# Kernel tuning notes

Measured on AMD Instinct MI355X. Metric: run time of the kernel, lower is better.

## Reference

```python
import jax, jax.numpy as jnp
import numpy as np
from jax.scipy.special import logsumexp

H = 128          # num_hidden_feature
L = 3            # num_layers (E3II/EGCL stack)
FL, FP = 16, 27  # ligand / pocket atom feature dims
NL, NP = 20000, 30000
EL, EP = 160000, 240000
B = 8            # graphs in the batch


def setup_inputs() -> dict:
    key = jax.random.key(0)
    ks = list(jax.random.split(key, 32))
    it = iter(ks)
    def rn(shape, s=0.05):
        return jax.random.normal(next(it), shape, jnp.float32) * s
    inp = {
        'ligand_x': jax.random.normal(next(it), (NL, FL), jnp.float32),
        'pocket_x': jax.random.normal(next(it), (NP, FP), jnp.float32),
        'ligand_pos': jax.random.normal(next(it), (NL, 3), jnp.float32),
        'pocket_pos': jax.random.normal(next(it), (NP, 3), jnp.float32),
        'Wl_emb': rn((FL, H)), 'bl_emb': rn((H,)),
        'Wp_emb': rn((FP, H)), 'bp_emb': rn((H,)),
        # per-layer EGCL params, stacked: axis0 = {0: ligand(l2l), 1: pocket(p2p)}, axis1 = layer
        'We1': rn((2, L, 2 * H + 1, H)), 'be1': rn((2, L, H)),
        'We2': rn((2, L, H, H)), 'be2': rn((2, L, H)),
        'Wx': rn((2, L, H, 1)), 'bx': rn((2, L, 1)),
        'Wh1': rn((2, L, 2 * H, H)), 'bh1': rn((2, L, H)),
        'Wh2': rn((2, L, H, H)), 'bh2': rn((2, L, H)),
        # NextType dense head: linspace(128,1,4) -> [128,85,43,1]
        'Wd1': rn((H, 85)), 'bd1': rn((85,)),
        'Wd2': rn((85, 43)), 'bd2': rn((43,)),
        'Wd3': rn((43, 1)), 'bd3': rn((1,)),
        'l2l_edge_index': jax.random.randint(next(it), (2, EL), 0, NL).astype(jnp.int32),
        'p2p_edge_index': jax.random.randint(next(it), (2, EP), 0, NP).astype(jnp.int32),
        'ligand_batch': jnp.sort(jax.random.randint(next(it), (NL,), 0, B)).astype(jnp.int32),
    }
    return inp


def _egcl(h, x, src, dst, We1, be1, We2, be2, Wx, bx, Wh1, bh1, Wh2, bh2):
    """One equivariant graph conv layer (gather -> edge MLP -> scatter)."""
    n = h.shape[0]
    rel = x[dst] - x[src]                                 # [E,3]
    d2 = jnp.sum(rel * rel, axis=-1, keepdims=True)        # [E,1]
    e_in = jnp.concatenate([h[dst], h[src], d2], axis=-1)  # [E,2H+1]
    m = jax.nn.silu(e_in @ We1 + be1)
    m = jax.nn.silu(m @ We2 + be2)                        # [E,H]
    coef = m @ Wx + bx                                     # [E,1]
    agg_x = jax.ops.segment_sum(rel * coef, dst, num_segments=n)
    deg = jax.ops.segment_sum(jnp.ones((dst.shape[0], 1), h.dtype), dst, num_segments=n)
    x = x + agg_x / jnp.maximum(deg, 1.0)                  # mean-normalized coord update
    agg_m = jax.ops.segment_sum(m, dst, num_segments=n)    # [N,H]
    upd = jax.nn.silu(jnp.concatenate([h, agg_m], axis=-1) @ Wh1 + bh1) @ Wh2 + bh2
    return h + upd, x


def reference(ligand_x, pocket_x, ligand_pos, pocket_pos,
              Wl_emb, bl_emb, Wp_emb, bp_emb,
              We1, be1, We2, be2, Wx, bx, Wh1, bh1, Wh2, bh2,
              Wd1, bd1, Wd2, bd2, Wd3, bd3,
              l2l_edge_index, p2p_edge_index, ligand_batch):
    # node embeddings (Embedding.l_node_emb / p_node_emb)
    hl = ligand_x @ Wl_emb + bl_emb
    hp = pocket_x @ Wp_emb + bp_emb
    xl, xp = ligand_pos, pocket_pos
    ls, ld = l2l_edge_index[0], l2l_edge_index[1]
    ps, pd = p2p_edge_index[0], p2p_edge_index[1]
    for l in range(L):
        hl, xl = _egcl(hl, xl, ls, ld, We1[0, l], be1[0, l], We2[0, l], be2[0, l],
                       Wx[0, l], bx[0, l], Wh1[0, l], bh1[0, l], Wh2[0, l], bh2[0, l])
        hp, xp = _egcl(hp, xp, ps, pd, We1[1, l], be1[1, l], We2[1, l], be2[1, l],
                       Wx[1, l], bx[1, l], Wh1[1, l], bh1[1, l], Wh2[1, l], bh2[1, l])
    # NextType head on ligand nodes: embedding(eye(FL)) == Wl_emb (+ bias)
    embed_type = Wl_emb + bl_emb                          # [FL,H]
    mul = embed_type[None, :, :] * hl[:, None, :]          # [NL,FL,H]
    t = jax.nn.silu(mul @ Wd1 + bd1)
    t = jax.nn.silu(t @ Wd2 + bd2)
    t = (t @ Wd3 + bd3)[..., 0]                            # [NL,FL]
    lg = jax.nn.log_softmax(t, axis=-1)
    agg = jax.ops.segment_sum(lg, ligand_batch, num_segments=B)  # [B,FL]
    return agg - logsumexp(agg, axis=-1, keepdims=True)
```

## Files before the change

kernel.cpp:

```cpp
#include <hip/hip_runtime.h>
#include <hip/hip_bf16.h>
#include <math.h>

typedef __attribute__((ext_vector_type(4))) float f4;
typedef __attribute__((ext_vector_type(4))) float f32x4;
typedef __attribute__((ext_vector_type(8))) short s8;
typedef __attribute__((ext_vector_type(4))) short s4;

#define H 128
#define NLAYERS 3
#define FLIG 16
#define FPOC 27
#define NLIG 20000
#define NPOC 30000
#define ELIG 160000
#define EPOC 240000
#define NB 8

#define EPB 128
#define NBLK_EL (ELIG/EPB)
#define NBLK_EP (EPOC/EPB)
#define NBLK_NL ((NLIG+31)/32)
#define NBLK_NP ((NPOC+31)/32)

#define G1S (8*8*64*8)
#define G2S (4*8*64*8)
#define W1FS (4*6*64*8)
#define WD2S (3*3*64*8)

__device__ __forceinline__ float silu_f(float v){
  return v * __builtin_amdgcn_rcpf(1.0f + __expf(-v));
}
__device__ __forceinline__ unsigned short f2bf(float v){
  __hip_bfloat16 b = __float2bfloat16(v);
  return *reinterpret_cast<unsigned short*>(&b);
}
__device__ __forceinline__ float bf2f(unsigned short u){
  unsigned int x = ((unsigned int)u) << 16;
  return __uint_as_float(x);
}
__device__ __forceinline__ int xcd_swz(int bid, int nwg){
  int q = nwg >> 3, r = nwg & 7;
  int x = bid & 7, w = bid >> 3;
  return (x < r) ? (x*(q+1) + w) : (r*(q+1) + (x-r)*q + w);
}

__global__ void k_embed2(const float* __restrict__ lx, const float* __restrict__ px,
                         const float* __restrict__ lpos, const float* __restrict__ ppos,
                         const float* __restrict__ Wl, const float* __restrict__ bl,
                         const float* __restrict__ Wp, const float* __restrict__ bp,
                         float* __restrict__ hl, unsigned short* __restrict__ hbl,
                         float* __restrict__ hp, unsigned short* __restrict__ hbp,
                         float* __restrict__ xl, float* __restrict__ xp){
  int bid = blockIdx.x;
  int g = (bid < NLIG/2) ? 0 : 1;
  int nb = (g ? bid - NLIG/2 : bid) * 2;
  const float* x  = g ? px : lx;
  const float* W  = g ? Wp : Wl;
  const float* b  = g ? bp : bl;
  float* h = g ? hp : hl;
  unsigned short* hb = g ? hbp : hbl;
  int F = g ? FPOC : FLIG;
  int tid = threadIdx.x;
  int n = nb + (tid >> 7);
  int j = tid & 127;
  float acc = b[j];
  for (int k = 0; k < F; k++) acc += x[n*F + k] * W[k*H + j];
  h[(size_t)n*H + j] = acc;
  hb[(size_t)n*H + j] = f2bf(acc);
  if (tid < 6){
    const float* pos = g ? ppos : lpos;
    float* xd = g ? xp : xl;
    xd[(size_t)nb*3 + tid] = pos[(size_t)nb*3 + tid];
  }
}

__global__ void k_hist2(const int* __restrict__ ldst, const int* __restrict__ pdst,
                        int* __restrict__ deg_l, int* __restrict__ deg_p){
  int e = blockIdx.x*256 + threadIdx.x;
  if (e < ELIG) atomicAdd(&deg_l[ldst[e]], 1);
  else if (e < ELIG+EPOC) atomicAdd(&deg_p[pdst[e-ELIG]], 1);
}

__global__ void k_scan2(const int* __restrict__ deg_l, int* __restrict__ offs_l,
                        const int* __restrict__ deg_p, int* __restrict__ offs_p){
  __shared__ int part[1024];
  const int* deg = blockIdx.x ? deg_p : deg_l;
  int* offs = blockIdx.x ? offs_p : offs_l;
  int N = blockIdx.x ? NPOC : NLIG;
  int E = blockIdx.x ? EPOC : ELIG;
  int t = threadIdx.x;
  int chunk = (N + 1023) >> 10;
  int b0 = t*chunk;
  int b1 = b0 + chunk; if (b1 > N) b1 = N;
  int s = 0;
  for (int i = b0; i < b1; i++) s += deg[i];
  part[t] = s;
  __syncthreads();
  for (int off = 1; off < 1024; off <<= 1){
    int v = (t >= off) ? part[t-off] : 0;
    __syncthreads();
    part[t] += v;
    __syncthreads();
  }
  int run = part[t] - s;
  for (int i = b0; i < b1; i++){ offs[i] = run; run += deg[i]; }
  if (t == 1023) offs[N] = E;
}

__global__ void k_sort2(const int* __restrict__ lsrc, const int* __restrict__ ldst,
                        const int* __restrict__ psrc, const int* __restrict__ pdst,
                        const int* __restrict__ offs_l, const int* __restrict__ offs_p,
                        int* __restrict__ cur_l, int* __restrict__ cur_p,
                        int* __restrict__ ssrc_l, int* __restrict__ sdst_l,
                        int* __restrict__ ssrc_p, int* __restrict__ sdst_p){
  int e = blockIdx.x*256 + threadIdx.x;
  if (e < ELIG){
    int d = ldst[e];
    int p = offs_l[d] + atomicAdd(&cur_l[d], 1);
    ssrc_l[p] = lsrc[e]; sdst_l[p] = d;
  } else if (e < ELIG+EPOC){
    int ee = e - ELIG;
    int d = pdst[ee];
    int p = offs_p[d] + atomicAdd(&cur_p[d], 1);
    ssrc_p[p] = psrc[ee]; sdst_p[p] = d;
  }
}

__global__ void k_pack(const float* __restrict__ We1, const float* __restrict__ We2,
                       const float* __restrict__ Wh1, const float* __restrict__ Wh2,
                       const float* __restrict__ Wl, const float* __restrict__ bl,
                       const float* __restrict__ Wd1, const float* __restrict__ Wd2,
                       unsigned short* __restrict__ We1p, unsigned short* __restrict__ We2p,
                       unsigned short* __restrict__ Wh1p, unsigned short* __restrict__ Wh2p,
                       unsigned short* __restrict__ W1p, unsigned short* __restrict__ Wd2p)
{
  int idx = blockIdx.x*256 + threadIdx.x;
  const int nWe1 = 6*G1S, nWe2 = 6*G2S, nWh1 = 6*G1S, nWh2 = 6*G2S, nW1 = 16*W1FS, nWd2 = WD2S;
  int i = idx;
  if (i < nWe1){
    int j = i&7, l = (i>>3)&63, t = (i>>9)&7, ks = (i>>12)&7, g = i>>15;
    int k = 32*ks + 8*(l>>4) + j, col = 16*t + (l&15);
    We1p[i] = f2bf(We1[((size_t)g*257 + k)*H + col]);
    return;
  }
  i -= nWe1;
  if (i < nWe2){
    int j = i&7, l = (i>>3)&63, t = (i>>9)&7, ks = (i>>12)&3, g = i>>14;
    int k = 32*ks + 8*(l>>4) + j, col = 16*t + (l&15);
    We2p[i] = f2bf(We2[((size_t)g*H + k)*H + col]);
    return;
  }
  i -= nWe2;
  if (i < nWh1){
    int j = i&7, l = (i>>3)&63, t = (i>>9)&7, ks = (i>>12)&7, g = i>>15;
    int k = 32*ks + 8*(l>>4) + j, col = 16*t + (l&15);
    Wh1p[i] = f2bf(Wh1[((size_t)g*256 + k)*H + col]);
    return;
  }
  i -= nWh1;
  if (i < nWh2){
    int j = i&7, l = (i>>3)&63, t = (i>>9)&7, ks = (i>>12)&3, g = i>>14;
    int k = 32*ks + 8*(l>>4) + j, col = 16*t + (l&15);
    Wh2p[i] = f2bf(Wh2[((size_t)g*H + k)*H + col]);
    return;
  }
  i -= nWh2;
  if (i < nW1){
    int f = i / W1FS, r = i % W1FS;
    int ks = r / (6*512), r2 = r % (6*512);
    int t = r2 / 512, l = (r2 % 512) >> 3, j = r2 & 7;
    int k = 32*ks + 8*(l>>4) + j, col = 16*t + (l&15);
    float v = 0.f;
    if (col < 85) v = (Wl[f*H + k] + bl[k]) * Wd1[k*85 + col];
    W1p[i] = f2bf(v);
    return;
  }
  i -= nW1;
  if (i < nWd2){
    int ks = i / (3*512), r2 = i % (3*512);
    int t = r2 / 512, l = (r2 % 512) >> 3, j = r2 & 7;
    int k = 32*ks + 8*(l>>4) + j, col = 16*t + (l&15);
    float v = 0.f;
    if (k < 85 && col < 43) v = Wd2[k*43 + col];
    Wd2p[i] = f2bf(v);
  }
}

__global__ __launch_bounds__(256, 3) void k_edge_f(
    const unsigned short* __restrict__ hb_l, const unsigned short* __restrict__ hb_p,
    const float* __restrict__ x_l, const float* __restrict__ x_p,
    const int* __restrict__ ssrc_l, const int* __restrict__ sdst_l,
    const int* __restrict__ ssrc_p, const int* __restrict__ sdst_p,
    const unsigned short* __restrict__ We1pb, const float* __restrict__ We1b,
    const float* __restrict__ be1b,
    const unsigned short* __restrict__ We2pb, const float* __restrict__ be2b,
    const float* __restrict__ Wxb, const float* __restrict__ bxb,
    unsigned short* __restrict__ m2e_l, float* __restrict__ relcf_l,
    unsigned short* __restrict__ m2e_p, float* __restrict__ relcf_p,
    int layer)
{
  __shared__ __align__(16) unsigned short m_lds[128*136];
  __shared__ float relS[128][3];
  __shared__ float d2S[128];
  __shared__ int sI[128], dI[128];
  unsigned short* m2t = m_lds;

  int tid = threadIdx.x;
  int bid = xcd_swz(blockIdx.x, NBLK_EL + NBLK_EP);
  int g = (bid < NBLK_EL) ? 0 : 1;
  int e0 = (g ? bid - NBLK_EL : bid) * EPB;
  const unsigned short* hb = g ? hb_p : hb_l;
  const float* x = g ? x_p : x_l;
  const int* ssrc = g ? ssrc_p : ssrc_l;
  const int* sdst = g ? sdst_p : sdst_l;
  unsigned short* m2e = g ? m2e_p : m2e_l;
  float* relcf = g ? relcf_p : relcf_l;
  int gl = g*NLAYERS + layer;
  const unsigned short* We1p = We1pb + (size_t)gl*G1S;
  const unsigned short* We2p = We2pb + (size_t)gl*G2S;
  const float* We1r256 = We1b + ((size_t)gl*257 + 256)*H;
  const float* be1 = be1b + (size_t)gl*H;
  const float* be2 = be2b + (size_t)gl*H;
  const float* Wx = Wxb + (size_t)gl*H;

  int lane = tid & 63, wave = tid >> 6;
  int c = lane & 15, q = lane >> 4;

  if (lane < 32){
    int e = wave*32 + lane;
    int s = ssrc[e0+e], d = sdst[e0+e];
    sI[e] = s; dI[e] = d;
    float rx = x[d*3+0]-x[s*3+0];
    float ry = x[d*3+1]-x[s*3+1];
    float rz = x[d*3+2]-x[s*3+2];
    relS[e][0]=rx; relS[e][1]=ry; relS[e][2]=rz;
    d2S[e] = rx*rx+ry*ry+rz*rz;
  }

  int eA = wave*32 + c;
  int eB = eA + 16;
  const unsigned short* pD0 = hb + (size_t)dI[eA]*H + q*8;
  const unsigned short* pS0 = hb + (size_t)sI[eA]*H + q*8;
  const unsigned short* pD1 = hb + (size_t)dI[eB]*H + q*8;
  const unsigned short* pS1 = hb + (size_t)sI[eB]*H + q*8;

  s8 af0[8], af1[8];
  #pragma unroll
  for (int ks=0; ks<4; ks++){
    af0[ks]   = *(const s8*)(pD0 + ks*32);
    af0[4+ks] = *(const s8*)(pS0 + ks*32);
    af1[ks]   = *(const s8*)(pD1 + ks*32);
    af1[4+ks] = *(const s8*)(pS1 + ks*32);
  }

  f32x4 acc0[8], acc1[8];
  #pragma unroll
  for (int t=0;t<8;t++){ acc0[t] = (f32x4){0.f,0.f,0.f,0.f}; acc1[t] = (f32x4){0.f,0.f,0.f,0.f}; }
  const s8* B1 = (const s8*)We1p;
  #pragma unroll
  for (int ks=0; ks<8; ks++){
    const s8* bp = B1 + (ks*8)*64 + lane;
    #pragma unroll
    for (int t=0;t<8;t++){
      s8 B = bp[t*64];
      acc0[t] = __builtin_amdgcn_mfma_f32_16x16x32_bf16(af0[ks], B, acc0[t], 0,0,0);
      acc1[t] = __builtin_amdgcn_mfma_f32_16x16x32_bf16(af1[ks], B, acc1[t], 0,0,0);
    }
  }

  int er0 = wave*32 + 4*q;
  int er1 = er0 + 16;
  float d20[4], d21[4];
  #pragma unroll
  for (int i=0;i<4;i++){ d20[i] = d2S[er0+i]; d21[i] = d2S[er1+i]; }
  #pragma unroll
  for (int t=0;t<8;t++){
    int j2 = 16*t + c;
    float w256 = We1r256[j2], bias = be1[j2];
    s4 mv0, mv1;
    #pragma unroll
    for (int i=0;i<4;i++){
      mv0[i] = (short)f2bf(silu_f(acc0[t][i] + d20[i]*w256 + bias));
      mv1[i] = (short)f2bf(silu_f(acc1[t][i] + d21[i]*w256 + bias));
    }
    *(s4*)&m_lds[136*j2 + er0] = mv0;
    *(s4*)&m_lds[136*j2 + er1] = mv1;
  }

  #pragma unroll
  for (int t=0;t<8;t++){ acc0[t] = (f32x4){0.f,0.f,0.f,0.f}; acc1[t] = (f32x4){0.f,0.f,0.f,0.f}; }
  const s8* B2 = (const s8*)We2p;
  #pragma unroll
  for (int ks=0; ks<4; ks++){
    s8 a20, a21;
    int base = 136*(32*ks + 8*q) + wave*32 + c;
    #pragma unroll
    for (int j=0;j<8;j++){
      a20[j] = (short)m_lds[base + 136*j];
      a21[j] = (short)m_lds[base + 16 + 136*j];
    }
    const s8* bp = B2 + (ks*8)*64 + lane;
    #pragma unroll
    for (int t=0;t<8;t++){
      s8 B = bp[t*64];
      acc0[t] = __builtin_amdgcn_mfma_f32_16x16x32_bf16(a20, B, acc0[t], 0,0,0);
      acc1[t] = __builtin_amdgcn_mfma_f32_16x16x32_bf16(a21, B, acc1[t], 0,0,0);
    }
  }
  __syncthreads();

  float pp0[4] = {0.f,0.f,0.f,0.f};
  float pp1[4] = {0.f,0.f,0.f,0.f};
  #pragma unroll
  for (int t=0;t<8;t++){
    int j2 = 16*t + c;
    float b2v = be2[j2], wxv = Wx[j2];
    #pragma unroll
    for (int i=0;i<4;i++){
      float v0 = silu_f(acc0[t][i] + b2v);
      float v1 = silu_f(acc1[t][i] + b2v);
      pp0[i] += v0*wxv;
      pp1[i] += v1*wxv;
      m2t[(er0+i)*136 + j2] = f2bf(v0);
      m2t[(er1+i)*136 + j2] = f2bf(v1);
    }
  }
  #pragma unroll
  for (int off=1; off<16; off<<=1){
    #pragma unroll
    for (int i=0;i<4;i++){
      pp0[i] += __shfl_xor(pp0[i], off, 64);
      pp1[i] += __shfl_xor(pp1[i], off, 64);
    }
  }
  if (c == 0){
    float bxv = bxb[gl];
    #pragma unroll
    for (int i=0;i<4;i++){
      int e = er0 + i;
      float cf = pp0[i] + bxv;
      float* rp = relcf + (size_t)(e0+e)*3;
      rp[0] = relS[e][0]*cf; rp[1] = relS[e][1]*cf; rp[2] = relS[e][2]*cf;
      e = er1 + i;
      cf = pp1[i] + bxv;
      rp = relcf + (size_t)(e0+e)*3;
      rp[0] = relS[e][0]*cf; rp[1] = relS[e][1]*cf; rp[2] = relS[e][2]*cf;
    }
  }

  {
    int e = wave*32 + (lane >> 1), cb = (lane & 1) * 64;
    const s8* sp = (const s8*)&m2t[e*136 + cb];
    s8* dp = (s8*)(m2e + (size_t)(e0+e)*H + cb);
    #pragma unroll
    for (int s2=0; s2<8; s2++) dp[s2] = sp[s2];
  }
}

__global__ __launch_bounds__(128, 4) void k_node_f(
    float* __restrict__ h_l, unsigned short* __restrict__ hb_l, float* __restrict__ x_l,
    float* __restrict__ h_p, unsigned short* __restrict__ hb_p, float* __restrict__ x_p,
    const unsigned short* __restrict__ m2e_l, const float* __restrict__ relcf_l,
    const unsigned short* __restrict__ m2e_p, const float* __restrict__ relcf_p,
    const int* __restrict__ offs_l, const int* __restrict__ offs_p,
    const unsigned short* __restrict__ Wh1pb, const float* __restrict__ bh1b,
    const unsigned short* __restrict__ Wh2pb, const float* __restrict__ bh2b,
    int layer)
{
  __shared__ __align__(16) unsigned short aggS[32*136];
  __shared__ __align__(16) unsigned short u_lds[128*36];
  __shared__ float rcS[32][3];
  __shared__ int degS[32];

  int tid = threadIdx.x;
  int bid = xcd_swz(blockIdx.x, NBLK_NL + NBLK_NP);
  int g = (bid < NBLK_NL) ? 0 : 1;
  int nb0 = (g ? bid - NBLK_NL : bid) * 32;
  int N = g ? NPOC : NLIG;
  float* h = g ? h_p : h_l;
  unsigned short* hbm = g ? hb_p : hb_l;
  float* x = g ? x_p : x_l;
  const unsigned short* m2e = g ? m2e_p : m2e_l;
  const float* relcf = g ? relcf_p : relcf_l;
  const int* offs = g ? offs_p : offs_l;
  int gl = g*NLAYERS + layer;
  const unsigned short* Wh1p = Wh1pb + (size_t)gl*G1S;
  const unsigned short* Wh2p = Wh2pb + (size_t)gl*G2S;
  const float* bh1 = bh1b + (size_t)gl*H;
  const float* bh2 = bh2b + (size_t)gl*H;

  int lane = tid & 63, wave = tid >> 6;

  {
    int nloc = tid >> 2, cb = (tid & 3) * 32;
    int gn = nb0 + nloc;
    int gna = (gn < N) ? gn : (N-1);
    int o0 = offs[gna], o1 = offs[gna+1];
    float sums[32];
    #pragma unroll
    for (int k=0;k<32;k++) sums[k] = 0.f;
    float rc0=0.f, rc1=0.f, rc2=0.f;
    bool rc_owner = (tid & 3) == 0;
    for (int e = o0; e < o1; e++){
      const unsigned short* mp = m2e + (size_t)e*H + cb;
      #pragma unroll
      for (int s2=0; s2<4; s2++){
        s8 v = *(const s8*)(mp + s2*8);
        #pragma unroll
        for (int j=0;j<8;j++)
          sums[s2*8+j] += bf2f((unsigned short)v[j]);
      }
      if (rc_owner){
        const float* rp = relcf + (size_t)e*3;
        rc0 += rp[0]; rc1 += rp[1]; rc2 += rp[2];
      }
    }
    unsigned short* ap = &aggS[nloc*136 + cb];
    #pragma unroll
    for (int s2=0; s2<4; s2++){
      s8 vv;
      #pragma unroll
      for (int j=0;j<8;j++) vv[j] = (short)f2bf(sums[s2*8+j]);
      *(s8*)(ap + s2*8) = vv;
    }
    if (rc_owner){
      rcS[nloc][0] = rc0; rcS[nloc][1] = rc1; rcS[nloc][2] = rc2;
      degS[nloc] = o1 - o0;
    }
  }

  if (lane < 48){
    int nn = wave*16 + lane/3, cc = lane - (lane/3)*3;
    int gn = nb0 + nn;
    if (gn < N){
      float dv = (float)degS[nn]; if (dv < 1.f) dv = 1.f;
      x[(size_t)gn*3 + cc] += rcS[nn][cc] / dv;
    }
  }

  int c = lane & 15, q = lane >> 4;
  int node = nb0 + wave*16 + c;
  int na = node < N ? node : N-1;
  int nloc2 = wave*16 + c;

  s8 af[8];
  #pragma unroll
  for (int ks=0; ks<4; ks++)
    af[ks] = *(const s8*)(hbm + (size_t)na*H + ks*32 + q*8);
  #pragma unroll
  for (int ks=4; ks<8; ks++)
    af[ks] = *(const s8*)&aggS[nloc2*136 + (ks-4)*32 + q*8];

  f32x4 acc[8];
  #pragma unroll
  for (int t=0;t<8;t++) acc[t] = (f32x4){0.f,0.f,0.f,0.f};
  const s8* B1 = (const s8*)Wh1p;
  #pragma unroll
  for (int ks=0; ks<8; ks++){
    const s8* bp = B1 + (ks*8)*64 + lane;
    #pragma unroll
    for (int t=0;t<8;t++)
      acc[t] = __builtin_amdgcn_mfma_f32_16x16x32_bf16(af[ks], bp[t*64], acc[t], 0,0,0);
  }

  int er0 = wave*16 + 4*q;
  #pragma unroll
  for (int t=0;t<8;t++){
    int j2 = 16*t + c;
    float b1 = bh1[j2];
    s4 mv;
    #pragma unroll
    for (int i=0;i<4;i++) mv[i] = (short)f2bf(silu_f(acc[t][i] + b1));
    *(s4*)&u_lds[36*j2 + er0] = mv;
  }

  f32x4 acc2[8];
  #pragma unroll
  for (int t=0;t<8;t++) acc2[t] = (f32x4){0.f,0.f,0.f,0.f};
  const s8* B2 = (const s8*)Wh2p;
  #pragma unroll
  for (int ks=0; ks<4; ks++){
    s8 a2;
    int base = 36*(32*ks + 8*q) + wave*16 + c;
    #pragma unroll
    for (int j=0;j<8;j++) a2[j] = (short)u_lds[base + 36*j];
    const s8* bp = B2 + (ks*8)*64 + lane;
    #pragma unroll
    for (int t=0;t<8;t++)
      acc2[t] = __builtin_amdgcn_mfma_f32_16x16x32_bf16(a2, bp[t*64], acc2[t], 0,0,0);
  }

  #pragma unroll
  for (int t=0;t<8;t++){
    int j2 = 16*t + c;
    float b2 = bh2[j2];
    #pragma unroll
    for (int i=0;i<4;i++){
      int gr = nb0 + wave*16 + 4*q + i;
      if (gr < N){
        size_t off = (size_t)gr*H + j2;
        float hv = h[off] + acc2[t][i] + b2;
        h[off] = hv;
        hbm[off] = f2bf(hv);
      }
    }
  }
}

__global__ __launch_bounds__(512, 2) void k_head3(
    const unsigned short* __restrict__ hb, const int* __restrict__ batch,
    const unsigned short* __restrict__ W1p, const float* __restrict__ bd1,
    const unsigned short* __restrict__ Wd2p, const float* __restrict__ bd2,
    const float* __restrict__ Wd3, const float* __restrict__ bd3,
    float* __restrict__ agg, int N)
{
  __shared__ __align__(16) unsigned short t1tr[96*132];
  __shared__ float t3s[32][18];
  __shared__ float lgs[32][18];
  __shared__ int bI[32];

  int tid = threadIdx.x;
  int nb0 = blockIdx.x * 32;
  int lane = tid & 63, wave = tid >> 6;
  int pair = wave >> 1, sub = wave & 1;
  int c = lane & 15, q = lane >> 4;

  int node = nb0 + sub*16 + c;
  int na = node < N ? node : N-1;

  s8 ah[4];
  #pragma unroll
  for (int ks=0; ks<4; ks++)
    ah[ks] = *(const s8*)(hb + (size_t)na*H + ks*32 + q*8);

  float b1c[6];
  #pragma unroll
  for (int t=0;t<6;t++){ int col=16*t+c; b1c[t] = (col<85) ? bd1[col] : 0.f; }
  float b2c[3], w3c[3];
  #pragma unroll
  for (int t=0;t<3;t++){
    int col=16*t+c;
    b2c[t] = (col<43) ? bd2[col] : 0.f;
    w3c[t] = (col<43) ? Wd3[col] : 0.f;
  }
  float bd3v = bd3[0];
  int rbase = wave*16;
  int er0 = rbase + 4*q;

  for (int fi=0; fi<4; fi++){
    int f = pair + 4*fi;
    const s8* B1 = (const s8*)W1p + f*(W1FS/8);
    f32x4 acc[6];
    #pragma unroll
    for (int t=0;t<6;t++) acc[t] = (f32x4){0.f,0.f,0.f,0.f};
    #pragma unroll
    for (int ks=0; ks<4; ks++){
      #pragma unroll
      for (int t=0;t<6;t++)
        acc[t] = __builtin_amdgcn_mfma_f32_16x16x32_bf16(ah[ks], B1[(ks*6+t)*64+lane], acc[t], 0,0,0);
    }
    #pragma unroll
    for (int t=0;t<6;t++){
      int j2 = 16*t + c;
      s4 mv;
      #pragma unroll
      for (int i=0;i<4;i++) mv[i] = (short)f2bf(silu_f(acc[t][i] + b1c[t]));
      *(s4*)&t1tr[132*j2 + er0] = mv;
    }
    f32x4 acc2[3];
    #pragma unroll
    for (int t=0;t<3;t++) acc2[t] = (f32x4){0.f,0.f,0.f,0.f};
    const s8* B2 = (const s8*)Wd2p;
    #pragma unroll
    for (int ks=0; ks<3; ks++){
      s8 a2;
      int base = 132*(32*ks + 8*q) + rbase + c;
      #pragma unroll
      for (int j=0;j<8;j++) a2[j] = (short)t1tr[base + 132*j];
      #pragma unroll
      for (int t=0;t<3;t++)
        acc2[t] = __builtin_amdgcn_mfma_f32_16x16x32_bf16(a2, B2[(ks*3+t)*64+lane], acc2[t], 0,0,0);
    }
    float pp[4] = {0.f,0.f,0.f,0.f};
    #pragma unroll
    for (int t=0;t<3;t++){
      #pragma unroll
      for (int i=0;i<4;i++) pp[i] += silu_f(acc2[t][i] + b2c[t]) * w3c[t];
    }
    #pragma unroll
    for (int off=1; off<16; off<<=1){
      #pragma unroll
      for (int i=0;i<4;i++) pp[i] += __shfl_xor(pp[i], off, 64);
    }
    if (c == 0){
      #pragma unroll
      for (int i=0;i<4;i++) t3s[sub*16 + 4*q + i][f] = pp[i] + bd3v;
    }
  }
  __syncthreads();

  if (tid < 32){
    int n = nb0 + tid;
    bool valid = n < N;
    bI[tid] = batch[valid ? n : (N-1)];
    if (valid){
      float m = t3s[tid][0];
      #pragma unroll
      for (int i=1;i<16;i++) m = fmaxf(m, t3s[tid][i]);
      float s = 0.f;
      #pragma unroll
      for (int i=0;i<16;i++) s += __expf(t3s[tid][i] - m);
      float ls = __logf(s);
      #pragma unroll
      for (int i=0;i<16;i++) lgs[tid][i] = t3s[tid][i] - m - ls;
    } else {
      #pragma unroll
      for (int i=0;i<16;i++) lgs[tid][i] = 0.f;
    }
  }
  __syncthreads();

  if (tid < 16){
    int f = tid;
    float acc = 0.f; int run = bI[0];
    for (int n = 0; n < 32; n++){
      int b = bI[n];
      if (b != run){ atomicAdd(&agg[run*16 + f], acc); acc = 0.f; run = b; }
      acc += lgs[n][f];
    }
    atomicAdd(&agg[run*16 + f], acc);
  }
}

__global__ void k_final(const float* __restrict__ agg, float* __restrict__ out){
  int tid = threadIdx.x;
  float vv = agg[tid];
  float m = vv;
  #pragma unroll
  for (int off = 1; off < 16; off <<= 1) m = fmaxf(m, __shfl_xor(m, off, 64));
  float s = __expf(vv - m);
  #pragma unroll
  for (int off = 1; off < 16; off <<= 1) s += __shfl_xor(s, off, 64);
  out[tid] = vv - m - __logf(s);
}

extern "C" void kernel_launch(void* const* d_in, const int* in_sizes, int n_in,
                              void* d_out, int out_size, void* d_ws, size_t ws_size,
                              hipStream_t stream)
{
  const float* ligand_x   = (const float*)d_in[0];
  const float* pocket_x   = (const float*)d_in[1];
  const float* ligand_pos = (const float*)d_in[2];
  const float* pocket_pos = (const float*)d_in[3];
  const float* Wl_emb = (const float*)d_in[4];
  const float* bl_emb = (const float*)d_in[5];
  const float* Wp_emb = (const float*)d_in[6];
  const float* bp_emb = (const float*)d_in[7];
  const float* We1 = (const float*)d_in[8];
  const float* be1 = (const float*)d_in[9];
  const float* We2 = (const float*)d_in[10];
  const float* be2 = (const float*)d_in[11];
  const float* Wx  = (const float*)d_in[12];
  const float* bx  = (const float*)d_in[13];
  const float* Wh1 = (const float*)d_in[14];
  const float* bh1 = (const float*)d_in[15];
  const float* Wh2 = (const float*)d_in[16];
  const float* bh2 = (const float*)d_in[17];
  const float* Wd1 = (const float*)d_in[18];
  const float* bd1 = (const float*)d_in[19];
  const float* Wd2 = (const float*)d_in[20];
  const float* bd2 = (const float*)d_in[21];
  const float* Wd3 = (const float*)d_in[22];
  const float* bd3 = (const float*)d_in[23];
  const int* l2l    = (const int*)d_in[24];
  const int* p2p    = (const int*)d_in[25];
  const int* lbatch = (const int*)d_in[26];

  char* w = (char*)d_ws;
  auto alloc = [&](size_t bytes)->char*{
    char* p = w; w += (bytes + 255) & ~(size_t)255; return p;
  };
  float* hl    = (float*)alloc((size_t)NLIG*H*4);
  float* hp    = (float*)alloc((size_t)NPOC*H*4);
  unsigned short* hbl = (unsigned short*)alloc((size_t)NLIG*H*2);
  unsigned short* hbp = (unsigned short*)alloc((size_t)NPOC*H*2);
  float* xl    = (float*)alloc((size_t)NLIG*3*4);
  float* xp    = (float*)alloc((size_t)NPOC*3*4);
  int* offs_l = (int*)alloc((size_t)(NLIG+1)*4);
  int* offs_p = (int*)alloc((size_t)(NPOC+1)*4);
  int* ssrc_l = (int*)alloc((size_t)ELIG*4);
  int* sdst_l = (int*)alloc((size_t)ELIG*4);
  int* ssrc_p = (int*)alloc((size_t)EPOC*4);
  int* sdst_p = (int*)alloc((size_t)EPOC*4);
  unsigned short* We1p = (unsigned short*)alloc((size_t)6*G1S*2);
  unsigned short* We2p = (unsigned short*)alloc((size_t)6*G2S*2);
  unsigned short* Wh1p = (unsigned short*)alloc((size_t)6*G1S*2);
  unsigned short* Wh2p = (unsigned short*)alloc((size_t)6*G2S*2);
  unsigned short* W1p  = (unsigned short*)alloc((size_t)16*W1FS*2);
  unsigned short* Wd2p = (unsigned short*)alloc((size_t)WD2S*2);
  unsigned short* m2e_l = (unsigned short*)alloc((size_t)ELIG*H*2);
  unsigned short* m2e_p = (unsigned short*)alloc((size_t)EPOC*H*2);
  float* relcf_l = (float*)alloc((size_t)ELIG*3*4);
  float* relcf_p = (float*)alloc((size_t)EPOC*3*4);
  char* zbase = w;
  int* deg_l = (int*)alloc((size_t)NLIG*4);
  int* deg_p = (int*)alloc((size_t)NPOC*4);
  int* cur_l = (int*)alloc((size_t)NLIG*4);
  int* cur_p = (int*)alloc((size_t)NPOC*4);
  float* aggB = (float*)alloc((size_t)NB*16*4);
  size_t zsize = (size_t)(w - zbase);

  hipMemsetAsync(zbase, 0, zsize, stream);

  const int* lsrc = l2l;          const int* ldst = l2l + ELIG;
  const int* psrc = p2p;          const int* pdst = p2p + EPOC;

  k_embed2<<<NLIG/2 + NPOC/2, 256, 0, stream>>>(ligand_x, pocket_x, ligand_pos, pocket_pos,
      Wl_emb, bl_emb, Wp_emb, bp_emb, hl, hbl, hp, hbp, xl, xp);
  k_hist2<<<(ELIG+EPOC+255)/256, 256, 0, stream>>>(ldst, pdst, deg_l, deg_p);
  k_scan2<<<2, 1024, 0, stream>>>(deg_l, offs_l, deg_p, offs_p);
  k_sort2<<<(ELIG+EPOC+255)/256, 256, 0, stream>>>(lsrc, ldst, psrc, pdst,
      offs_l, offs_p, cur_l, cur_p, ssrc_l, sdst_l, ssrc_p, sdst_p);
  {
    int npack = 6*G1S + 6*G2S + 6*G1S + 6*G2S + 16*W1FS + WD2S;
    k_pack<<<(npack+255)/256, 256, 0, stream>>>(We1, We2, Wh1, Wh2,
        Wl_emb, bl_emb, Wd1, Wd2, We1p, We2p, Wh1p, Wh2p, W1p, Wd2p);
  }

  for (int l = 0; l < NLAYERS; l++){
    k_edge_f<<<NBLK_EL + NBLK_EP, 256, 0, stream>>>(hbl, hbp, xl, xp,
        ssrc_l, sdst_l, ssrc_p, sdst_p,
        We1p, We1, be1, We2p, be2, Wx, bx,
        m2e_l, relcf_l, m2e_p, relcf_p, l);
    k_node_f<<<NBLK_NL + NBLK_NP, 128, 0, stream>>>(hl, hbl, xl, hp, hbp, xp,
        m2e_l, relcf_l, m2e_p, relcf_p, offs_l, offs_p,
        Wh1p, bh1, Wh2p, bh2, l);
  }

  k_head3<<<(NLIG+31)/32, 512, 0, stream>>>(hbl, lbatch, W1p, bd1, Wd2p, bd2,
                                            Wd3, bd3, aggB, NLIG);
  k_final<<<1, 128, 0, stream>>>(aggB, (float*)d_out);
}
```

Measured before the change: 660.4 us.

## Fuse edge MLP and node update into one per-layer kernel with LDS aggregation

Merges the edge-message kernel and the node-update kernel into a single per-layer kernel. Each wave owns 16 destination nodes, walks their dst-sorted edges in chunks of 32, and accumulates messages and coordinate terms with LDS atomics. This drops the materialised per-edge message and relcf buffers in global memory and one launch per layer. Because blocks now read neighbour features while others write, h and x are ping-ponged between A/B buffers. The cost is per-wave serial edge chunks with padded partial chunks, LDS atomics, and load imbalance across nodes with different degrees.

```diff
diff --git a/kernel.cpp b/kernel.cpp
--- a/kernel.cpp
+++ b/kernel.cpp
@@ -17,9 +17,6 @@
 #define EPOC 240000
 #define NB 8
 
-#define EPB 128
-#define NBLK_EL (ELIG/EPB)
-#define NBLK_EP (EPOC/EPB)
 #define NBLK_NL ((NLIG+31)/32)
 #define NBLK_NP ((NPOC+31)/32)
 
@@ -34,10 +31,6 @@
 __device__ __forceinline__ unsigned short f2bf(float v){
   __hip_bfloat16 b = __float2bfloat16(v);
   return *reinterpret_cast<unsigned short*>(&b);
-}
-__device__ __forceinline__ float bf2f(unsigned short u){
-  unsigned int x = ((unsigned int)u) << 16;
-  return __uint_as_float(x);
 }
 __device__ __forceinline__ int xcd_swz(int bid, int nwg){
   int q = nwg >> 3, r = nwg & 7;
@@ -187,35 +180,47 @@
   }
 }
 
-__global__ __launch_bounds__(256, 3) void k_edge_f(
-    const unsigned short* __restrict__ hb_l, const unsigned short* __restrict__ hb_p,
-    const float* __restrict__ x_l, const float* __restrict__ x_p,
+__global__ __launch_bounds__(128, 2) void k_layer_f(
+    const float* __restrict__ hi_l, const unsigned short* __restrict__ hbi_l,
+    const float* __restrict__ xi_l,
+    float* __restrict__ ho_l, unsigned short* __restrict__ hbo_l, float* __restrict__ xo_l,
+    const float* __restrict__ hi_p, const unsigned short* __restrict__ hbi_p,
+    const float* __restrict__ xi_p,
+    float* __restrict__ ho_p, unsigned short* __restrict__ hbo_p, float* __restrict__ xo_p,
     const int* __restrict__ ssrc_l, const int* __restrict__ sdst_l,
     const int* __restrict__ ssrc_p, const int* __restrict__ sdst_p,
+    const int* __restrict__ offs_l, const int* __restrict__ offs_p,
     const unsigned short* __restrict__ We1pb, const float* __restrict__ We1b,
     const float* __restrict__ be1b,
     const unsigned short* __restrict__ We2pb, const float* __restrict__ be2b,
     const float* __restrict__ Wxb, const float* __restrict__ bxb,
-    unsigned short* __restrict__ m2e_l, float* __restrict__ relcf_l,
-    unsigned short* __restrict__ m2e_p, float* __restrict__ relcf_p,
+    const unsigned short* __restrict__ Wh1pb, const float* __restrict__ bh1b,
+    const unsigned short* __restrict__ Wh2pb, const float* __restrict__ bh2b,
     int layer)
 {
-  __shared__ __align__(16) unsigned short m_lds[128*136];
-  __shared__ float relS[128][3];
-  __shared__ float d2S[128];
-  __shared__ int sI[128], dI[128];
-  unsigned short* m2t = m_lds;
+  __shared__ __align__(16) unsigned short m_chunk[2][128*36];
+  __shared__ __align__(16) float aggS[2][16*132];
+  __shared__ float rcW[2][16][3];
+  __shared__ float relW[2][32][3];
+  __shared__ float d2W[2][32];
+  __shared__ int dIw[2][32];
+  __shared__ int sIw[2][32];
+  __shared__ __align__(16) unsigned short u_lds[128*36];
 
   int tid = threadIdx.x;
-  int bid = xcd_swz(blockIdx.x, NBLK_EL + NBLK_EP);
-  int g = (bid < NBLK_EL) ? 0 : 1;
-  int e0 = (g ? bid - NBLK_EL : bid) * EPB;
-  const unsigned short* hb = g ? hb_p : hb_l;
-  const float* x = g ? x_p : x_l;
+  int bid = xcd_swz(blockIdx.x, NBLK_NL + NBLK_NP);
+  int g = (bid < NBLK_NL) ? 0 : 1;
+  int nb0 = (g ? bid - NBLK_NL : bid) * 32;
+  int N = g ? NPOC : NLIG;
+  const float* hi = g ? hi_p : hi_l;
+  const unsigned short* hbi = g ? hbi_p : hbi_l;
+  const float* xi = g ? xi_p : xi_l;
+  float* ho = g ? ho_p : ho_l;
+  unsigned short* hbo = g ? hbo_p : hbo_l;
+  float* xo = g ? xo_p : xo_l;
   const int* ssrc = g ? ssrc_p : ssrc_l;
   const int* sdst = g ? sdst_p : sdst_l;
-  unsigned short* m2e = g ? m2e_p : m2e_l;
-  float* relcf = g ? relcf_p : relcf_l;
+  const int* offs = g ? offs_p : offs_l;
   int gl = g*NLAYERS + layer;
   const unsigned short* We1p = We1pb + (size_t)gl*G1S;
   const unsigned short* We2p = We2pb + (size_t)gl*G2S;
@@ -223,248 +228,212 @@
   const float* be1 = be1b + (size_t)gl*H;
   const float* be2 = be2b + (size_t)gl*H;
   const float* Wx = Wxb + (size_t)gl*H;
-
-  int lane = tid & 63, wave = tid >> 6;
-  int c = lane & 15, q = lane >> 4;
-
-  if (lane < 32){
-    int e = wave*32 + lane;
-    int s = ssrc[e0+e], d = sdst[e0+e];
-    sI[e] = s; dI[e] = d;
-    float rx = x[d*3+0]-x[s*3+0];
-    float ry = x[d*3+1]-x[s*3+1];
-    float rz = x[d*3+2]-x[s*3+2];
-    relS[e][0]=rx; relS[e][1]=ry; relS[e][2]=rz;
-    d2S[e] = rx*rx+ry*ry+rz*rz;
-  }
-
-  int eA = wave*32 + c;
-  int eB = eA + 16;
-  const unsigned short* pD0 = hb + (size_t)dI[eA]*H + q*8;
-  const unsigned short* pS0 = hb + (size_t)sI[eA]*H + q*8;
-  const unsigned short* pD1 = hb + (size_t)dI[eB]*H + q*8;
-  const unsigned short* pS1 = hb + (size_t)sI[eB]*H + q*8;
-
-  s8 af0[8], af1[8];
-  #pragma unroll
-  for (int ks=0; ks<4; ks++){
-    af0[ks]   = *(const s8*)(pD0 + ks*32);
-    af0[4+ks] = *(const s8*)(pS0 + ks*32);
-    af1[ks]   = *(const s8*)(pD1 + ks*32);
-    af1[4+ks] = *(const s8*)(pS1 + ks*32);
-  }
-
-  f32x4 acc0[8], acc1[8];
-  #pragma unroll
-  for (int t=0;t<8;t++){ acc0[t] = (f32x4){0.f,0.f,0.f,0.f}; acc1[t] = (f32x4){0.f,0.f,0.f,0.f}; }
-  const s8* B1 = (const s8*)We1p;
-  #pragma unroll
-  for (int ks=0; ks<8; ks++){
-    const s8* bp = B1 + (ks*8)*64 + lane;
-    #pragma unroll
-    for (int t=0;t<8;t++){
-      s8 B = bp[t*64];
-      acc0[t] = __builtin_amdgcn_mfma_f32_16x16x32_bf16(af0[ks], B, acc0[t], 0,0,0);
-      acc1[t] = __builtin_amdgcn_mfma_f32_16x16x32_bf16(af1[ks], B, acc1[t], 0,0,0);
-    }
-  }
-
-  int er0 = wave*32 + 4*q;
-  int er1 = er0 + 16;
-  float d20[4], d21[4];
-  #pragma unroll
-  for (int i=0;i<4;i++){ d20[i] = d2S[er0+i]; d21[i] = d2S[er1+i]; }
-  #pragma unroll
-  for (int t=0;t<8;t++){
-    int j2 = 16*t + c;
-    float w256 = We1r256[j2], bias = be1[j2];
-    s4 mv0, mv1;
-    #pragma unroll
-    for (int i=0;i<4;i++){
-      mv0[i] = (short)f2bf(silu_f(acc0[t][i] + d20[i]*w256 + bias));
-      mv1[i] = (short)f2bf(silu_f(acc1[t][i] + d21[i]*w256 + bias));
-    }
-    *(s4*)&m_lds[136*j2 + er0] = mv0;
-    *(s4*)&m_lds[136*j2 + er1] = mv1;
-  }
-
-  #pragma unroll
-  for (int t=0;t<8;t++){ acc0[t] = (f32x4){0.f,0.f,0.f,0.f}; acc1[t] = (f32x4){0.f,0.f,0.f,0.f}; }
-  const s8* B2 = (const s8*)We2p;
-  #pragma unroll
-  for (int ks=0; ks<4; ks++){
-    s8 a20, a21;
-    int base = 136*(32*ks + 8*q) + wave*32 + c;
-    #pragma unroll
-    for (int j=0;j<8;j++){
-      a20[j] = (short)m_lds[base + 136*j];
-      a21[j] = (short)m_lds[base + 16 + 136*j];
-    }
-    const s8* bp = B2 + (ks*8)*64 + lane;
-    #pragma unroll
-    for (int t=0;t<8;t++){
-      s8 B = bp[t*64];
-      acc0[t] = __builtin_amdgcn_mfma_f32_16x16x32_bf16(a20, B, acc0[t], 0,0,0);
-      acc1[t] = __builtin_amdgcn_mfma_f32_16x16x32_bf16(a21, B, acc1[t], 0,0,0);
-    }
-  }
-  __syncthreads();
-
-  float pp0[4] = {0.f,0.f,0.f,0.f};
-  float pp1[4] = {0.f,0.f,0.f,0.f};
-  #pragma unroll
-  for (int t=0;t<8;t++){
-    int j2 = 16*t + c;
-    float b2v = be2[j2], wxv = Wx[j2];
-    #pragma unroll
-    for (int i=0;i<4;i++){
-      float v0 = silu_f(acc0[t][i] + b2v);
-      float v1 = silu_f(acc1[t][i] + b2v);
-      pp0[i] += v0*wxv;
-      pp1[i] += v1*wxv;
-      m2t[(er0+i)*136 + j2] = f2bf(v0);
-      m2t[(er1+i)*136 + j2] = f2bf(v1);
-    }
-  }
-  #pragma unroll
-  for (int off=1; off<16; off<<=1){
-    #pragma unroll
-    for (int i=0;i<4;i++){
-      pp0[i] += __shfl_xor(pp0[i], off, 64);
-      pp1[i] += __shfl_xor(pp1[i], off, 64);
-    }
-  }
-  if (c == 0){
-    float bxv = bxb[gl];
-    #pragma unroll
-    for (int i=0;i<4;i++){
-      int e = er0 + i;
-      float cf = pp0[i] + bxv;
-      float* rp = relcf + (size_t)(e0+e)*3;
-      rp[0] = relS[e][0]*cf; rp[1] = relS[e][1]*cf; rp[2] = relS[e][2]*cf;
-      e = er1 + i;
-      cf = pp1[i] + bxv;
-      rp = relcf + (size_t)(e0+e)*3;
-      rp[0] = relS[e][0]*cf; rp[1] = relS[e][1]*cf; rp[2] = relS[e][2]*cf;
-    }
-  }
-
-  {
-    int e = wave*32 + (lane >> 1), cb = (lane & 1) * 64;
-    const s8* sp = (const s8*)&m2t[e*136 + cb];
-    s8* dp = (s8*)(m2e + (size_t)(e0+e)*H + cb);
-    #pragma unroll
-    for (int s2=0; s2<8; s2++) dp[s2] = sp[s2];
-  }
-}
-
-__global__ __launch_bounds__(128, 4) void k_node_f(
-    float* __restrict__ h_l, unsigned short* __restrict__ hb_l, float* __restrict__ x_l,
-    float* __restrict__ h_p, unsigned short* __restrict__ hb_p, float* __restrict__ x_p,
-    const unsigned short* __restrict__ m2e_l, const float* __restrict__ relcf_l,
-    const unsigned short* __restrict__ m2e_p, const float* __restrict__ relcf_p,
-    const int* __restrict__ offs_l, const int* __restrict__ offs_p,
-    const unsigned short* __restrict__ Wh1pb, const float* __restrict__ bh1b,
-    const unsigned short* __restrict__ Wh2pb, const float* __restrict__ bh2b,
-    int layer)
-{
-  __shared__ __align__(16) unsigned short aggS[32*136];
-  __shared__ __align__(16) unsigned short u_lds[128*36];
-  __shared__ float rcS[32][3];
-  __shared__ int degS[32];
-
-  int tid = threadIdx.x;
-  int bid = xcd_swz(blockIdx.x, NBLK_NL + NBLK_NP);
-  int g = (bid < NBLK_NL) ? 0 : 1;
-  int nb0 = (g ? bid - NBLK_NL : bid) * 32;
-  int N = g ? NPOC : NLIG;
-  float* h = g ? h_p : h_l;
-  unsigned short* hbm = g ? hb_p : hb_l;
-  float* x = g ? x_p : x_l;
-  const unsigned short* m2e = g ? m2e_p : m2e_l;
-  const float* relcf = g ? relcf_p : relcf_l;
-  const int* offs = g ? offs_p : offs_l;
-  int gl = g*NLAYERS + layer;
   const unsigned short* Wh1p = Wh1pb + (size_t)gl*G1S;
   const unsigned short* Wh2p = Wh2pb + (size_t)gl*G2S;
   const float* bh1 = bh1b + (size_t)gl*H;
   const float* bh2 = bh2b + (size_t)gl*H;
 
-  int lane = tid & 63, wave = tid >> 6;
-
-  {
-    int nloc = tid >> 2, cb = (tid & 3) * 32;
-    int gn = nb0 + nloc;
-    int gna = (gn < N) ? gn : (N-1);
-    int o0 = offs[gna], o1 = offs[gna+1];
-    float sums[32];
-    #pragma unroll
-    for (int k=0;k<32;k++) sums[k] = 0.f;
-    float rc0=0.f, rc1=0.f, rc2=0.f;
-    bool rc_owner = (tid & 3) == 0;
-    for (int e = o0; e < o1; e++){
-      const unsigned short* mp = m2e + (size_t)e*H + cb;
-      #pragma unroll
-      for (int s2=0; s2<4; s2++){
-        s8 v = *(const s8*)(mp + s2*8);
-        #pragma unroll
-        for (int j=0;j<8;j++)
-          sums[s2*8+j] += bf2f((unsigned short)v[j]);
+  int lane = tid & 63, wv = tid >> 6;
+  int c = lane & 15, q = lane >> 4;
+
+  for (int i = lane; i < 16*132; i += 64) aggS[wv][i] = 0.f;
+  if (lane < 48) rcW[wv][lane/3][lane - (lane/3)*3] = 0.f;
+
+  int gn0 = nb0 + wv*16;
+  int lo = gn0 < N ? gn0 : N;
+  int hi2 = gn0+16 < N ? gn0+16 : N;
+  int oa = offs[lo], ob = offs[hi2];
+  float bxv = bxb[gl];
+
+  for (int eb = oa; eb < ob; eb += 32){
+    if (lane < 32){
+      int eg = eb + lane;
+      int egc = eg < ob ? eg : ob-1;
+      int s = ssrc[egc], d = sdst[egc];
+      sIw[wv][lane] = s;
+      dIw[wv][lane] = d - gn0;
+      float rx = xi[d*3+0]-xi[s*3+0];
+      float ry = xi[d*3+1]-xi[s*3+1];
+      float rz = xi[d*3+2]-xi[s*3+2];
+      relW[wv][lane][0]=rx; relW[wv][lane][1]=ry; relW[wv][lane][2]=rz;
+      d2W[wv][lane] = rx*rx+ry*ry+rz*rz;
+    }
+    int dg0 = gn0 + dIw[wv][c],    sg0 = sIw[wv][c];
+    int dg1 = gn0 + dIw[wv][16+c], sg1 = sIw[wv][16+c];
+    const unsigned short* pD0 = hbi + (size_t)dg0*H + q*8;
+    const unsigned short* pS0 = hbi + (size_t)sg0*H + q*8;
+    const unsigned short* pD1 = hbi + (size_t)dg1*H + q*8;
+    const unsigned short* pS1 = hbi + (size_t)sg1*H + q*8;
+    s8 af0[8], af1[8];
+    #pragma unroll
+    for (int ks=0; ks<4; ks++){
+      af0[ks]   = *(const s8*)(pD0 + ks*32);
+      af0[4+ks] = *(const s8*)(pS0 + ks*32);
+      af1[ks]   = *(const s8*)(pD1 + ks*32);
+      af1[4+ks] = *(const s8*)(pS1 + ks*32);
+    }
+
+    f32x4 acc0[8], acc1[8];
+    #pragma unroll
+    for (int t=0;t<8;t++){ acc0[t] = (f32x4){0.f,0.f,0.f,0.f}; acc1[t] = (f32x4){0.f,0.f,0.f,0.f}; }
+    const s8* B1 = (const s8*)We1p;
+    #pragma unroll
+    for (int ks=0; ks<8; ks++){
+      const s8* bp = B1 + (ks*8)*64 + lane;
+      #pragma unroll
+      for (int t=0;t<8;t++){
+        s8 B = bp[t*64];
+        acc0[t] = __builtin_amdgcn_mfma_f32_16x16x32_bf16(af0[ks], B, acc0[t], 0,0,0);
+        acc1[t] = __builtin_amdgcn_mfma_f32_16x16x32_bf16(af1[ks], B, acc1[t], 0,0,0);
       }
-      if (rc_owner){
-        const float* rp = relcf + (size_t)e*3;
-        rc0 += rp[0]; rc1 += rp[1]; rc2 += rp[2];
+    }
+
+    int er0 = 4*q, er1 = 16 + 4*q;
+    float d20[4], d21[4];
+    #pragma unroll
+    for (int i=0;i<4;i++){ d20[i] = d2W[wv][er0+i]; d21[i] = d2W[wv][er1+i]; }
+    unsigned short* mw = &m_chunk[wv][0];
+    #pragma unroll
+    for (int t=0;t<8;t++){
+      int j2 = 16*t + c;
+      float w256 = We1r256[j2], bias = be1[j2];
+      s4 mv0, mv1;
+      #pragma unroll
+      for (int i=0;i<4;i++){
+        mv0[i] = (short)f2bf(silu_f(acc0[t][i] + d20[i]*w256 + bias));
+        mv1[i] = (short)f2bf(silu_f(acc1[t][i] + d21[i]*w256 + bias));
       }
-    }
-    unsigned short* ap = &aggS[nloc*136 + cb];
-    #pragma unroll
-    for (int s2=0; s2<4; s2++){
-      s8 vv;
-      #pragma unroll
-      for (int j=0;j<8;j++) vv[j] = (short)f2bf(sums[s2*8+j]);
-      *(s8*)(ap + s2*8) = vv;
-    }
-    if (rc_owner){
-      rcS[nloc][0] = rc0; rcS[nloc][1] = rc1; rcS[nloc][2] = rc2;
-      degS[nloc] = o1 - o0;
+      *(s4*)&mw[36*j2 + er0] = mv0;
+      *(s4*)&mw[36*j2 + er1] = mv1;
+    }
+
+    #pragma unroll
+    for (int t=0;t<8;t++){ acc0[t] = (f32x4){0.f,0.f,0.f,0.f}; acc1[t] = (f32x4){0.f,0.f,0.f,0.f}; }
+    const s8* B2 = (const s8*)We2p;
+    #pragma unroll
+    for (int ks=0; ks<4; ks++){
+      s8 a20, a21;
+      int base = 36*(32*ks + 8*q) + c;
+      #pragma unroll
+      for (int j=0;j<8;j++){
+        a20[j] = (short)mw[base + 36*j];
+        a21[j] = (short)mw[base + 16 + 36*j];
+      }
+      const s8* bp = B2 + (ks*8)*64 + lane;
+      #pragma unroll
+      for (int t=0;t<8;t++){
+        s8 B = bp[t*64];
+        acc0[t] = __builtin_amdgcn_mfma_f32_16x16x32_bf16(a20, B, acc0[t], 0,0,0);
+        acc1[t] = __builtin_amdgcn_mfma_f32_16x16x32_bf16(a21, B, acc1[t], 0,0,0);
+      }
+    }
+
+    int dl0[4], dl1[4];
+    float vm0[4], vm1[4];
+    #pragma unroll
+    for (int i=0;i<4;i++){
+      dl0[i] = dIw[wv][er0+i];
+      dl1[i] = dIw[wv][er1+i];
+      vm0[i] = (eb + er0 + i < ob) ? 1.f : 0.f;
+      vm1[i] = (eb + er1 + i < ob) ? 1.f : 0.f;
+    }
+    float pp0[4] = {0.f,0.f,0.f,0.f};
+    float pp1[4] = {0.f,0.f,0.f,0.f};
+    float* ag = &aggS[wv][0];
+    #pragma unroll
+    for (int t=0;t<8;t++){
+      int j2 = 16*t + c;
+      float b2v = be2[j2], wxv = Wx[j2];
+      float v0[4], v1[4];
+      #pragma unroll
+      for (int i=0;i<4;i++){
+        v0[i] = silu_f(acc0[t][i] + b2v);
+        v1[i] = silu_f(acc1[t][i] + b2v);
+        pp0[i] += v0[i]*wxv;
+        pp1[i] += v1[i]*wxv;
+      }
+      float s = v0[0]*vm0[0];
+      if (dl0[1]!=dl0[0]){ atomicAdd(&ag[dl0[0]*132 + j2], s); s = v0[1]*vm0[1]; } else s += v0[1]*vm0[1];
+      if (dl0[2]!=dl0[1]){ atomicAdd(&ag[dl0[1]*132 + j2], s); s = v0[2]*vm0[2]; } else s += v0[2]*vm0[2];
+      if (dl0[3]!=dl0[2]){ atomicAdd(&ag[dl0[2]*132 + j2], s); s = v0[3]*vm0[3]; } else s += v0[3]*vm0[3];
+      atomicAdd(&ag[dl0[3]*132 + j2], s);
+      s = v1[0]*vm1[0];
+      if (dl1[1]!=dl1[0]){ atomicAdd(&ag[dl1[0]*132 + j2], s); s = v1[1]*vm1[1]; } else s += v1[1]*vm1[1];
+      if (dl1[2]!=dl1[1]){ atomicAdd(&ag[dl1[1]*132 + j2], s); s = v1[2]*vm1[2]; } else s += v1[2]*vm1[2];
+      if (dl1[3]!=dl1[2]){ atomicAdd(&ag[dl1[2]*132 + j2], s); s = v1[3]*vm1[3]; } else s += v1[3]*vm1[3];
+      atomicAdd(&ag[dl1[3]*132 + j2], s);
+    }
+    #pragma unroll
+    for (int off=1; off<16; off<<=1){
+      #pragma unroll
+      for (int i=0;i<4;i++){
+        pp0[i] += __shfl_xor(pp0[i], off, 64);
+        pp1[i] += __shfl_xor(pp1[i], off, 64);
+      }
+    }
+    if (c == 0){
+      #pragma unroll
+      for (int i=0;i<4;i++){
+        int sl = er0 + i;
+        if (eb + sl < ob){
+          int dl = dIw[wv][sl];
+          float cf = pp0[i] + bxv;
+          atomicAdd(&rcW[wv][dl][0], relW[wv][sl][0]*cf);
+          atomicAdd(&rcW[wv][dl][1], relW[wv][sl][1]*cf);
+          atomicAdd(&rcW[wv][dl][2], relW[wv][sl][2]*cf);
+        }
+        sl = er1 + i;
+        if (eb + sl < ob){
+          int dl = dIw[wv][sl];
+          float cf = pp1[i] + bxv;
+          atomicAdd(&rcW[wv][dl][0], relW[wv][sl][0]*cf);
+          atomicAdd(&rcW[wv][dl][1], relW[wv][sl][1]*cf);
+          atomicAdd(&rcW[wv][dl][2], relW[wv][sl][2]*cf);
+        }
+      }
     }
   }
 
   if (lane < 48){
-    int nn = wave*16 + lane/3, cc = lane - (lane/3)*3;
-    int gn = nb0 + nn;
+    int nl = lane/3, cc = lane - nl*3;
+    int gn = gn0 + nl;
     if (gn < N){
-      float dv = (float)degS[nn]; if (dv < 1.f) dv = 1.f;
-      x[(size_t)gn*3 + cc] += rcS[nn][cc] / dv;
-    }
-  }
-
-  int c = lane & 15, q = lane >> 4;
-  int node = nb0 + wave*16 + c;
+      int dvi = offs[gn+1] - offs[gn];
+      float dv = dvi < 1 ? 1.f : (float)dvi;
+      xo[(size_t)gn*3 + cc] = xi[(size_t)gn*3 + cc] + rcW[wv][nl][cc]*__builtin_amdgcn_rcpf(dv);
+    }
+  }
+
+  int node = gn0 + c;
   int na = node < N ? node : N-1;
-  int nloc2 = wave*16 + c;
 
   s8 af[8];
   #pragma unroll
   for (int ks=0; ks<4; ks++)
-    af[ks] = *(const s8*)(hbm + (size_t)na*H + ks*32 + q*8);
-  #pragma unroll
-  for (int ks=4; ks<8; ks++)
-    af[ks] = *(const s8*)&aggS[nloc2*136 + (ks-4)*32 + q*8];
+    af[ks] = *(const s8*)(hbi + (size_t)na*H + ks*32 + q*8);
+  #pragma unroll
+  for (int ks=4; ks<8; ks++){
+    const float* am = &aggS[wv][c*132 + (ks-4)*32 + q*8];
+    f4 a0 = *(const f4*)am, a1 = *(const f4*)(am+4);
+    s8 p;
+    #pragma unroll
+    for (int jj=0;jj<4;jj++){ p[jj] = (short)f2bf(a0[jj]); p[4+jj] = (short)f2bf(a1[jj]); }
+    af[ks] = p;
+  }
 
   f32x4 acc[8];
   #pragma unroll
   for (int t=0;t<8;t++) acc[t] = (f32x4){0.f,0.f,0.f,0.f};
-  const s8* B1 = (const s8*)Wh1p;
+  const s8* B1n = (const s8*)Wh1p;
   #pragma unroll
   for (int ks=0; ks<8; ks++){
-    const s8* bp = B1 + (ks*8)*64 + lane;
+    const s8* bp = B1n + (ks*8)*64 + lane;
     #pragma unroll
     for (int t=0;t<8;t++)
       acc[t] = __builtin_amdgcn_mfma_f32_16x16x32_bf16(af[ks], bp[t*64], acc[t], 0,0,0);
   }
 
-  int er0 = wave*16 + 4*q;
+  int nr0 = wv*16 + 4*q;
   #pragma unroll
   for (int t=0;t<8;t++){
     int j2 = 16*t + c;
@@ -472,20 +441,20 @@
     s4 mv;
     #pragma unroll
     for (int i=0;i<4;i++) mv[i] = (short)f2bf(silu_f(acc[t][i] + b1));
-    *(s4*)&u_lds[36*j2 + er0] = mv;
+    *(s4*)&u_lds[36*j2 + nr0] = mv;
   }
 
   f32x4 acc2[8];
   #pragma unroll
   for (int t=0;t<8;t++) acc2[t] = (f32x4){0.f,0.f,0.f,0.f};
-  const s8* B2 = (const s8*)Wh2p;
+  const s8* B2n = (const s8*)Wh2p;
   #pragma unroll
   for (int ks=0; ks<4; ks++){
     s8 a2;
-    int base = 36*(32*ks + 8*q) + wave*16 + c;
+    int base = 36*(32*ks + 8*q) + wv*16 + c;
     #pragma unroll
     for (int j=0;j<8;j++) a2[j] = (short)u_lds[base + 36*j];
-    const s8* bp = B2 + (ks*8)*64 + lane;
+    const s8* bp = B2n + (ks*8)*64 + lane;
     #pragma unroll
     for (int t=0;t<8;t++)
       acc2[t] = __builtin_amdgcn_mfma_f32_16x16x32_bf16(a2, bp[t*64], acc2[t], 0,0,0);
@@ -497,12 +466,12 @@
     float b2 = bh2[j2];
     #pragma unroll
     for (int i=0;i<4;i++){
-      int gr = nb0 + wave*16 + 4*q + i;
+      int gr = gn0 + 4*q + i;
       if (gr < N){
         size_t off = (size_t)gr*H + j2;
-        float hv = h[off] + acc2[t][i] + b2;
-        h[off] = hv;
-        hbm[off] = f2bf(hv);
+        float hv = hi[off] + acc2[t][i] + b2;
+        ho[off] = hv;
+        hbo[off] = f2bf(hv);
       }
     }
   }
@@ -681,12 +650,18 @@
   auto alloc = [&](size_t bytes)->char*{
     char* p = w; w += (bytes + 255) & ~(size_t)255; return p;
   };
-  float* hl    = (float*)alloc((size_t)NLIG*H*4);
-  float* hp    = (float*)alloc((size_t)NPOC*H*4);
-  unsigned short* hbl = (unsigned short*)alloc((size_t)NLIG*H*2);
-  unsigned short* hbp = (unsigned short*)alloc((size_t)NPOC*H*2);
-  float* xl    = (float*)alloc((size_t)NLIG*3*4);
-  float* xp    = (float*)alloc((size_t)NPOC*3*4);
+  float* hA_l = (float*)alloc((size_t)NLIG*H*4);
+  float* hB_l = (float*)alloc((size_t)NLIG*H*4);
+  float* hA_p = (float*)alloc((size_t)NPOC*H*4);
+  float* hB_p = (float*)alloc((size_t)NPOC*H*4);
+  unsigned short* hbA_l = (unsigned short*)alloc((size_t)NLIG*H*2);
+  unsigned short* hbB_l = (unsigned short*)alloc((size_t)NLIG*H*2);
+  unsigned short* hbA_p = (unsigned short*)alloc((size_t)NPOC*H*2);
+  unsigned short* hbB_p = (unsigned short*)alloc((size_t)NPOC*H*2);
+  float* xA_l = (float*)alloc((size_t)NLIG*3*4);
+  float* xB_l = (float*)alloc((size_t)NLIG*3*4);
+  float* xA_p = (float*)alloc((size_t)NPOC*3*4);
+  float* xB_p = (float*)alloc((size_t)NPOC*3*4);
   int* offs_l = (int*)alloc((size_t)(NLIG+1)*4);
   int* offs_p = (int*)alloc((size_t)(NPOC+1)*4);
   int* ssrc_l = (int*)alloc((size_t)ELIG*4);
@@ -699,10 +674,6 @@
   unsigned short* Wh2p = (unsigned short*)alloc((size_t)6*G2S*2);
   unsigned short* W1p  = (unsigned short*)alloc((size_t)16*W1FS*2);
   unsigned short* Wd2p = (unsigned short*)alloc((size_t)WD2S*2);
-  unsigned short* m2e_l = (unsigned short*)alloc((size_t)ELIG*H*2);
-  unsigned short* m2e_p = (unsigned short*)alloc((size_t)EPOC*H*2);
-  float* relcf_l = (float*)alloc((size_t)ELIG*3*4);
-  float* relcf_p = (float*)alloc((size_t)EPOC*3*4);
   char* zbase = w;
   int* deg_l = (int*)alloc((size_t)NLIG*4);
   int* deg_p = (int*)alloc((size_t)NPOC*4);
@@ -717,7 +688,7 @@
   const int* psrc = p2p;          const int* pdst = p2p + EPOC;
 
   k_embed2<<<NLIG/2 + NPOC/2, 256, 0, stream>>>(ligand_x, pocket_x, ligand_pos, pocket_pos,
-      Wl_emb, bl_emb, Wp_emb, bp_emb, hl, hbl, hp, hbp, xl, xp);
+      Wl_emb, bl_emb, Wp_emb, bp_emb, hA_l, hbA_l, hA_p, hbA_p, xA_l, xA_p);
   k_hist2<<<(ELIG+EPOC+255)/256, 256, 0, stream>>>(ldst, pdst, deg_l, deg_p);
   k_scan2<<<2, 1024, 0, stream>>>(deg_l, offs_l, deg_p, offs_p);
   k_sort2<<<(ELIG+EPOC+255)/256, 256, 0, stream>>>(lsrc, ldst, psrc, pdst,
@@ -729,16 +700,24 @@
   }
 
   for (int l = 0; l < NLAYERS; l++){
-    k_edge_f<<<NBLK_EL + NBLK_EP, 256, 0, stream>>>(hbl, hbp, xl, xp,
-        ssrc_l, sdst_l, ssrc_p, sdst_p,
+    bool odd = (l & 1);
+    const float* hi_l = odd ? hB_l : hA_l;        float* ho_l = odd ? hA_l : hB_l;
+    const float* hi_p = odd ? hB_p : hA_p;        float* ho_p = odd ? hA_p : hB_p;
+    const unsigned short* hbi_l = odd ? hbB_l : hbA_l;
+    unsigned short* hbo_l = odd ? hbA_l : hbB_l;
+    const unsigned short* hbi_p = odd ? hbB_p : hbA_p;
+    unsigned short* hbo_p = odd ? hbA_p : hbB_p;
+    const float* xi_l = odd ? xB_l : xA_l;        float* xo_l = odd ? xA_l : xB_l;
+    const float* xi_p = odd ? xB_p : xA_p;        float* xo_p = odd ? xA_p : xB_p;
+    k_layer_f<<<NBLK_NL + NBLK_NP, 128, 0, stream>>>(
+        hi_l, hbi_l, xi_l, ho_l, hbo_l, xo_l,
+        hi_p, hbi_p, xi_p, ho_p, hbo_p, xo_p,
+        ssrc_l, sdst_l, ssrc_p, sdst_p, offs_l, offs_p,
         We1p, We1, be1, We2p, be2, Wx, bx,
-        m2e_l, relcf_l, m2e_p, relcf_p, l);
-    k_node_f<<<NBLK_NL + NBLK_NP, 128, 0, stream>>>(hl, hbl, xl, hp, hbp, xp,
-        m2e_l, relcf_l, m2e_p, relcf_p, offs_l, offs_p,
         Wh1p, bh1, Wh2p, bh2, l);
   }
 
-  k_head3<<<(NLIG+31)/32, 512, 0, stream>>>(hbl, lbatch, W1p, bd1, Wd2p, bd2,
+  k_head3<<<(NLIG+31)/32, 512, 0, stream>>>(hbB_l, lbatch, W1p, bd1, Wd2p, bd2,
                                             Wd3, bd3, aggB, NLIG);
   k_final<<<1, 128, 0, stream>>>(aggB, (float*)d_out);
 }
```

Measured after the change: 1.482 ms. 2.24x slower.
